# Optimization experiments

Measured on AMD Instinct MI355X. Metric: run time of the kernel, lower is better.

The kernel has to match this reference:

```python
import jax, jax.numpy as jnp
import numpy as np

VOCAB, NUM_TAGS, EMB, HID = 30000, 20, 200, 128
B, S = 128, 512


def setup_inputs() -> dict:
    key = jax.random.key(0)
    ks = jax.random.split(key, 13)
    sentence = jax.random.randint(ks[0], (B, S), 0, VOCAB)
    tags = jax.random.randint(ks[1], (B, S), 0, NUM_TAGS)
    lengths = jax.random.randint(ks[2], (B,), 1, S + 1)
    mask = jnp.arange(S)[None, :] < lengths[:, None]  # [B,S] bool, mask[:,0] all True
    sc = 0.1
    return {
        "sentence": sentence,
        "tags": tags,
        "mask": mask,
        "embedding": jax.random.normal(ks[3], (VOCAB, EMB), jnp.float32) * sc,
        "W_ih": jax.random.normal(ks[4], (4 * HID, EMB), jnp.float32) * sc,
        "W_hh": jax.random.normal(ks[5], (4 * HID, HID), jnp.float32) * sc,
        "b_ih": jax.random.normal(ks[6], (4 * HID,), jnp.float32) * sc,
        "b_hh": jax.random.normal(ks[7], (4 * HID,), jnp.float32) * sc,
        "W_dec": jax.random.normal(ks[8], (NUM_TAGS, HID), jnp.float32) * sc,
        "b_dec": jax.random.normal(ks[9], (NUM_TAGS,), jnp.float32) * sc,
        "start_trans": jax.random.normal(ks[10], (NUM_TAGS,), jnp.float32) * sc,
        "end_trans": jax.random.normal(ks[11], (NUM_TAGS,), jnp.float32) * sc,
        "trans": jax.random.normal(ks[12], (NUM_TAGS, NUM_TAGS), jnp.float32) * sc,
    }


def _lstm(embeds, W_ih, W_hh, b_ih, b_hh):
    # torch nn.LSTM, single layer, batch_first, zero init state; gate order i,f,g,o
    b = embeds.shape[0]
    h0 = jnp.zeros((b, HID), embeds.dtype)
    x = jnp.swapaxes(embeds, 0, 1)  # [S,B,E]
    xg = jnp.einsum('sbe,ge->sbg', x, W_ih) + b_ih + b_hh  # input projections, [S,B,4H]

    def step(carry, xg_t):
        h, c = carry
        g = xg_t + h @ W_hh.T
        i, f, gg, o = jnp.split(g, 4, axis=-1)
        c = jax.nn.sigmoid(f) * c + jax.nn.sigmoid(i) * jnp.tanh(gg)
        h = jax.nn.sigmoid(o) * jnp.tanh(c)
        return (h, c), h

    _, hs = jax.lax.scan(step, (h0, h0), xg)
    return jnp.swapaxes(hs, 0, 1)  # [B,S,H]


def _crf_nll_mean(emissions, tags, mask, start_trans, end_trans, trans):
    # torchcrf.CRF negative log likelihood, reduction='mean' (mean over batch)
    b = emissions.shape[0]
    ems = jnp.swapaxes(emissions, 0, 1)          # [S,B,T]
    tgs = jnp.swapaxes(tags, 0, 1)               # [S,B]
    msk = jnp.swapaxes(mask, 0, 1).astype(emissions.dtype)  # [S,B]
    bidx = jnp.arange(b)

    # numerator: score of the gold path
    num0 = start_trans[tgs[0]] + ems[0, bidx, tgs[0]]

    def nstep(score, inp):
        em, tag, ptag, m = inp
        return score + (trans[ptag, tag] + em[bidx, tag]) * m, None

    num, _ = jax.lax.scan(nstep, num0, (ems[1:], tgs[1:], tgs[:-1], msk[1:]))
    last_idx = mask.sum(axis=1).astype(jnp.int32) - 1
    num = num + end_trans[tags[bidx, last_idx]]

    # denominator: forward algorithm (log partition)
    sc0 = start_trans[None, :] + ems[0]  # [B,T]

    def dstep(score, inp):
        em, m = inp
        nxt = jax.nn.logsumexp(score[:, :, None] + trans[None] + em[:, None, :], axis=1)
        return jnp.where(m[:, None] > 0, nxt, score), None

    sc, _ = jax.lax.scan(dstep, sc0, (ems[1:], msk[1:]))
    den = jax.nn.logsumexp(sc + end_trans[None, :], axis=1)
    return -jnp.mean(num - den)


def reference(sentence, tags, mask, embedding, W_ih, W_hh, b_ih, b_hh,
              W_dec, b_dec, start_trans, end_trans, trans):
    embeds = embedding[sentence]                           # [B,S,E]
    lstm_out = _lstm(embeds, W_ih, W_hh, b_ih, b_hh)       # [B,S,H]
    emissions = jnp.einsum('bsh,th->bst', lstm_out, W_dec) + b_dec  # [B,S,T]
    # dropout treated as identity (eval-mode reference)
    return _crf_nll_mean(emissions, tags, mask, start_trans, end_trans, trans)
```

## Files before the change

kernel.cpp:

```cpp
#include <hip/hip_runtime.h>
#include <hip/hip_bf16.h>
#include <hip/hip_fp16.h>
#include <math.h>

#define B_ 128
#define S_ 512
#define EMB_ 200
#define HID_ 128
#define NT_ 20
#define G4_ 512
#define KP_ 224

typedef _Float16 f16x2_t __attribute__((ext_vector_type(2)));
typedef short bf16x8 __attribute__((ext_vector_type(8)));
typedef float f32x4 __attribute__((ext_vector_type(4)));

#if __has_builtin(__builtin_amdgcn_fdot2)
#define FDOT2(a, b, c) __builtin_amdgcn_fdot2(__builtin_bit_cast(f16x2_t, (a)), \
                                              __builtin_bit_cast(f16x2_t, (b)), (c), false)
#else
static __device__ __forceinline__ float fdot2_fb(unsigned a, unsigned b, float c) {
    float alo = __half2float(__ushort_as_half((unsigned short)(a & 0xffffu)));
    float ahi = __half2float(__ushort_as_half((unsigned short)(a >> 16)));
    float blo = __half2float(__ushort_as_half((unsigned short)(b & 0xffffu)));
    float bhi = __half2float(__ushort_as_half((unsigned short)(b >> 16)));
    return c + alo * blo + ahi * bhi;
}
#define FDOT2(a, b, c) fdot2_fb((a), (b), (c))
#endif

__device__ __forceinline__ float bf2f(unsigned u) {
    union { unsigned u; float f; } cv;
    cv.u = u << 16;
    return cv.f;
}
__device__ __forceinline__ unsigned packh2(float a, float b) {
    return ((unsigned)__half_as_ushort(__float2half(b)) << 16)
         | (unsigned)__half_as_ushort(__float2half(a));
}
__device__ __forceinline__ unsigned short f2bf(float f) {
    __hip_bfloat16 h = __float2bfloat16(f);
    unsigned short u;
    __builtin_memcpy(&u, &h, 2);
    return u;
}

__global__ void k_detect(const unsigned char* mask, int* flag) {
    __shared__ int partial[4];
    int tid = threadIdx.x;
    int s = 0;
    for (int i = tid; i < B_ * S_; i += 256) {
        if (i & 3) s += mask[i];
    }
    for (int m = 32; m >= 1; m >>= 1) s += __shfl_xor(s, m);
    if ((tid & 63) == 0) partial[tid >> 6] = s;
    __syncthreads();
    if (tid == 0) {
        int tot = partial[0] + partial[1] + partial[2] + partial[3];
        flag[0] = (tot > 0) ? 1 : 0;
    }
}

__global__ void k_prep(const float* __restrict__ W_ih, const float* __restrict__ b_ih,
                       const float* __restrict__ b_hh, __hip_bfloat16* __restrict__ Wb,
                       float* __restrict__ biasb) {
    int i = blockIdx.x * 256 + threadIdx.x;
    if (i < G4_ * KP_) {
        int g = i / KP_, k = i - g * KP_;
        float v = (k < EMB_) ? W_ih[g * EMB_ + k] : 0.f;
        Wb[i] = __float2bfloat16(v);
    }
    if (i < G4_) biasb[i] = b_ih[i] + b_hh[i];
}

__global__ __launch_bounds__(256, 2) void k_xg(const int* __restrict__ sentence,
                                               const float* __restrict__ embedding,
                                               const __hip_bfloat16* __restrict__ Wb,
                                               const float* __restrict__ biasb,
                                               __hip_bfloat16* __restrict__ xg) {
    __shared__ short Bl[G4_ * 40];
    __shared__ short Al[32 * 40];
    __shared__ int ids_s[32];
    int tid = threadIdx.x;
    int m0 = blockIdx.x * 32;
    int lane = tid & 63;
    int gbase = (tid >> 6) * 128;
    if (tid < 32) ids_s[tid] = sentence[m0 + tid];
    __syncthreads();

    f32x4 acc0[8], acc1[8];
#pragma unroll
    for (int n = 0; n < 8; n++) {
        acc0[n] = (f32x4){0.f, 0.f, 0.f, 0.f};
        acc1[n] = (f32x4){0.f, 0.f, 0.f, 0.f};
    }
    int lrow = lane & 15, lk = lane >> 4;

    for (int c = 0; c < 7; c++) {
        int k0 = c * 32;
#pragma unroll
        for (int i = 0; i < 8; i++) {
            int idx = tid + 256 * i;
            int row = idx >> 2, q = idx & 3;
            uint4 v = *(const uint4*)((const short*)Wb + (size_t)row * KP_ + k0 + q * 8);
            *(uint4*)(Bl + row * 40 + q * 8) = v;
        }
#pragma unroll
        for (int i = 0; i < 2; i++) {
            int j = tid + 256 * i;
            int row = j >> 4, kp = j & 15;
            int k = k0 + kp * 2;
            const float* e = embedding + (size_t)ids_s[row] * EMB_;
            float v0 = (k < EMB_) ? e[k] : 0.f;
            float v1 = (k + 1 < EMB_) ? e[k + 1] : 0.f;
            unsigned u = (unsigned)f2bf(v0) | ((unsigned)f2bf(v1) << 16);
            *(unsigned*)(Al + row * 40 + kp * 2) = u;
        }
        __syncthreads();
        bf16x8 a0 = *(const bf16x8*)(Al + lrow * 40 + lk * 8);
        bf16x8 a1 = *(const bf16x8*)(Al + (lrow + 16) * 40 + lk * 8);
#pragma unroll
        for (int n = 0; n < 8; n++) {
            bf16x8 bfr = *(const bf16x8*)(Bl + (gbase + n * 16 + lrow) * 40 + lk * 8);
            acc0[n] = __builtin_amdgcn_mfma_f32_16x16x32_bf16(a0, bfr, acc0[n], 0, 0, 0);
            acc1[n] = __builtin_amdgcn_mfma_f32_16x16x32_bf16(a1, bfr, acc1[n], 0, 0, 0);
        }
        __syncthreads();
    }
    int rbase = m0 + lk * 4;
#pragma unroll
    for (int n = 0; n < 8; n++) {
        int g = gbase + n * 16 + lrow;
        float bv = biasb[g];
#pragma unroll
        for (int r = 0; r < 4; r++) {
            xg[(size_t)(rbase + r) * G4_ + g] = __float2bfloat16(acc0[n][r] + bv);
            xg[(size_t)(rbase + r + 16) * G4_ + g] = __float2bfloat16(acc1[n][r] + bv);
        }
    }
}

__global__ __launch_bounds__(1024) __attribute__((amdgpu_waves_per_eu(4, 4)))
void k_lstm(const __hip_bfloat16* __restrict__ xg,
            const float* __restrict__ W_hh,
            unsigned* __restrict__ h2_out) {
    __shared__ unsigned h2_lds[64];
    __shared__ float gate_lds[G4_];
    int b = blockIdx.x, tid = threadIdx.x;
    int g = tid >> 1;
    int half = tid & 1;

    unsigned w2[32];
    const float2* wrow = (const float2*)(W_hh + (size_t)g * HID_ + half * 64);
#pragma unroll
    for (int k = 0; k < 32; k++) {
        float2 f = wrow[k];
        w2[k] = packh2(f.x, f.y);
    }
#pragma unroll
    for (int k = 0; k < 32; k++) asm("" : "+v"(w2[k]));

    if (tid < 64) h2_lds[tid] = 0u;
    float c0 = 0.f, c1 = 0.f;
    const ushort* xgb = (const ushort*)(xg) + (size_t)b * S_ * G4_;
    unsigned* h2b = h2_out + (size_t)b * S_ * 64;
    int gt = g >> 7;
    __syncthreads();

    unsigned xr = xgb[g];
    for (int t = 0; t < S_; t++) {
        int tn = (t + 1 < S_) ? t + 1 : t;
        unsigned xr_next = xgb[(size_t)tn * G4_ + g];

        float acc = 0.f;
        const uint4* hb4 = (const uint4*)(h2_lds + (half << 5));
#pragma unroll
        for (int q = 0; q < 8; q++) {
            uint4 hh = hb4[q];
            acc = FDOT2(w2[4 * q + 0], hh.x, acc);
            acc = FDOT2(w2[4 * q + 1], hh.y, acc);
            acc = FDOT2(w2[4 * q + 2], hh.z, acc);
            acc = FDOT2(w2[4 * q + 3], hh.w, acc);
        }
        acc += __shfl_xor(acc, 1);
        if (half == 0) {
            float pre = bf2f(xr) + acc;
            float xs = (gt == 2) ? 2.f * pre : pre;
            xs = fminf(fmaxf(xs, -30.f), 30.f);
            float r = 1.f / (1.f + __expf(-xs));
            gate_lds[g] = (gt == 2) ? 2.f * r - 1.f : r;
        }
        __syncthreads();
        if (tid < 64) {
            int j = tid;
            float2 iv = *(const float2*)(gate_lds + 2 * j);
            float2 fv = *(const float2*)(gate_lds + 128 + 2 * j);
            float2 gv = *(const float2*)(gate_lds + 256 + 2 * j);
            float2 ov = *(const float2*)(gate_lds + 384 + 2 * j);
            c0 = fv.x * c0 + iv.x * gv.x;
            c1 = fv.y * c1 + iv.y * gv.y;
            float h0 = ov.x * (2.f / (1.f + __expf(-2.f * c0)) - 1.f);
            float h1 = ov.y * (2.f / (1.f + __expf(-2.f * c1)) - 1.f);
            unsigned pk = packh2(h0, h1);
            h2_lds[j] = pk;
            h2b[(size_t)t * 64 + j] = pk;
        }
        __syncthreads();
        xr = xr_next;
    }
}

__global__ __launch_bounds__(320) void k_em(const unsigned* __restrict__ h2,
                                            const float* __restrict__ W_dec,
                                            const float* __restrict__ b_dec,
                                            float* __restrict__ em) {
    int half = threadIdx.x / 160;
    int r = threadIdx.x % 160;
    int tag = r >> 3, l8 = r & 7;
    const float* wd = W_dec + tag * HID_ + l8 * 16;
    float ws[16];
#pragma unroll
    for (int q = 0; q < 16; q++) ws[q] = wd[q];
    float bd = b_dec[tag];
    int row0 = blockIdx.x * 16 + half * 8;
    for (int rp = 0; rp < 8; rp++) {
        int row = row0 + rp;
        const uint4* h4 = (const uint4*)(h2 + (size_t)row * 64 + l8 * 8);
        uint4 a = h4[0], bq = h4[1];
        unsigned hv[8] = {a.x, a.y, a.z, a.w, bq.x, bq.y, bq.z, bq.w};
        float pacc = 0.f;
#pragma unroll
        for (int q = 0; q < 8; q++) {
            float lo = __half2float(__ushort_as_half((unsigned short)(hv[q] & 0xffffu)));
            float hi = __half2float(__ushort_as_half((unsigned short)(hv[q] >> 16)));
            pacc += lo * ws[2 * q] + hi * ws[2 * q + 1];
        }
        pacc += __shfl_xor(pacc, 1);
        pacc += __shfl_xor(pacc, 2);
        pacc += __shfl_xor(pacc, 4);
        if (l8 == 0) em[(size_t)row * NT_ + tag] = pacc + bd;
    }
}

__global__ __launch_bounds__(64) void k_crf(const float* __restrict__ em,
                                            const int* __restrict__ tags,
                                            const void* __restrict__ mask,
                                            const int* __restrict__ flag,
                                            const float* __restrict__ start_trans,
                                            const float* __restrict__ end_trans,
                                            const float* __restrict__ trans,
                                            float* __restrict__ nll) {
    __shared__ float em_s[S_ * NT_];
    __shared__ float trans_s[NT_ * NT_];
    __shared__ int tags_s[S_];
    __shared__ unsigned char mask_s[S_];
    __shared__ __align__(16) float score_s[32];
    __shared__ float num_sh;

    int b = blockIdx.x;
    int lane = threadIdx.x;
    const float4* e4 = (const float4*)(em + (size_t)b * S_ * NT_);
    float4* s4 = (float4*)em_s;
    for (int i = lane; i < S_ * NT_ / 4; i += 64) s4[i] = e4[i];
    for (int i = lane; i < NT_ * NT_; i += 64) trans_s[i] = trans[i];
    for (int i = lane; i < S_; i += 64) tags_s[i] = tags[b * S_ + i];
    int fl = flag[0];
    for (int i = lane; i < S_; i += 64) {
        mask_s[i] = fl ? ((const unsigned char*)mask)[b * S_ + i]
                       : (unsigned char)(((const int*)mask)[b * S_ + i] != 0);
    }
    __syncthreads();

    float nsum = 0.f;
    int cnt = 0;
    for (int t = lane; t < S_; t += 64) cnt += mask_s[t];
    for (int t = 1 + lane; t < S_; t += 64) {
        if (mask_s[t]) {
            int tg = tags_s[t], pt = tags_s[t - 1];
            nsum += trans_s[pt * NT_ + tg] + em_s[t * NT_ + tg];
        }
    }
    for (int m = 32; m >= 1; m >>= 1) {
        nsum += __shfl_xor(nsum, m);
        cnt += __shfl_xor(cnt, m);
    }
    if (lane == 0) {
        int t0 = tags_s[0];
        num_sh = nsum + start_trans[t0] + em_s[t0] + end_trans[tags_s[cnt - 1]];
    }

    int tag = (lane < NT_) ? lane : NT_ - 1;
    float tcol[NT_];
#pragma unroll
    for (int p = 0; p < NT_; p++) tcol[p] = trans_s[p * NT_ + tag];
    float sc = start_trans[tag] + em_s[tag];
    if (lane < NT_) score_s[lane] = sc;
    __syncthreads();

    for (int t = 1; t < S_; t++) {
        const float4* q4 = (const float4*)score_s;
        float4 q0 = q4[0], q1 = q4[1], q2 = q4[2], q3 = q4[3], q5 = q4[4];
        float v[NT_] = {q0.x + tcol[0],  q0.y + tcol[1],  q0.z + tcol[2],  q0.w + tcol[3],
                        q1.x + tcol[4],  q1.y + tcol[5],  q1.z + tcol[6],  q1.w + tcol[7],
                        q2.x + tcol[8],  q2.y + tcol[9],  q2.z + tcol[10], q2.w + tcol[11],
                        q3.x + tcol[12], q3.y + tcol[13], q3.z + tcol[14], q3.w + tcol[15],
                        q5.x + tcol[16], q5.y + tcol[17], q5.z + tcol[18], q5.w + tcol[19]};
        float mx[NT_];
#pragma unroll
        for (int p = 0; p < NT_; p++) mx[p] = v[p];
#pragma unroll
        for (int n = NT_; n > 1; n = (n + 1) >> 1) {
#pragma unroll
            for (int i = 0; i < (n >> 1); i++) mx[i] = fmaxf(mx[i], mx[n - 1 - i]);
        }
        float ex[NT_];
#pragma unroll
        for (int p = 0; p < NT_; p++) ex[p] = __expf(v[p] - mx[0]);
#pragma unroll
        for (int n = NT_; n > 1; n = (n + 1) >> 1) {
#pragma unroll
            for (int i = 0; i < (n >> 1); i++) ex[i] += ex[n - 1 - i];
        }
        float nxt = mx[0] + __logf(ex[0]) + em_s[t * NT_ + tag];
        sc = mask_s[t] ? nxt : sc;
        __syncthreads();
        if (lane < NT_) score_s[lane] = sc;
        __syncthreads();
    }

    if (lane < NT_) score_s[lane] = sc + end_trans[tag];
    __syncthreads();
    if (lane == 0) {
        float m = score_s[0];
#pragma unroll
        for (int i = 1; i < NT_; i++) m = fmaxf(m, score_s[i]);
        float s = 0.f;
#pragma unroll
        for (int i = 0; i < NT_; i++) s += __expf(score_s[i] - m);
        nll[b] = (m + __logf(s)) - num_sh;
    }
}

__global__ void k_final(const float* __restrict__ nll, float* __restrict__ out) {
    __shared__ float sums[2];
    int tid = threadIdx.x;
    float v = nll[tid];
    for (int m = 32; m >= 1; m >>= 1) v += __shfl_xor(v, m);
    if ((tid & 63) == 0) sums[tid >> 6] = v;
    __syncthreads();
    if (tid == 0) out[0] = (sums[0] + sums[1]) * (1.f / (float)B_);
}

extern "C" void kernel_launch(void* const* d_in, const int* in_sizes, int n_in,
                              void* d_out, int out_size, void* d_ws, size_t ws_size,
                              hipStream_t stream) {
    const int* sentence = (const int*)d_in[0];
    const int* tags = (const int*)d_in[1];
    const void* mask = d_in[2];
    const float* embedding = (const float*)d_in[3];
    const float* W_ih = (const float*)d_in[4];
    const float* W_hh = (const float*)d_in[5];
    const float* b_ih = (const float*)d_in[6];
    const float* b_hh = (const float*)d_in[7];
    const float* W_dec = (const float*)d_in[8];
    const float* b_dec = (const float*)d_in[9];
    const float* start_trans = (const float*)d_in[10];
    const float* end_trans = (const float*)d_in[11];
    const float* trans = (const float*)d_in[12];

    char* ws = (char*)d_ws;
    int* flag = (int*)ws;
    __hip_bfloat16* xg = (__hip_bfloat16*)(ws + 256);
    size_t off = 256 + (size_t)B_ * S_ * G4_ * 2;
    float* em = (float*)(ws + off);
    off += (size_t)B_ * S_ * NT_ * 4;
    float* nllp = (float*)(ws + off);
    off += 512;
    unsigned* h2_out = (unsigned*)(ws + off);
    off += (size_t)B_ * S_ * 64 * 4;
    __hip_bfloat16* Wb = (__hip_bfloat16*)(ws + off);
    off += (size_t)G4_ * KP_ * 2;
    float* biasb = (float*)(ws + off);

    k_detect<<<1, 256, 0, stream>>>((const unsigned char*)mask, flag);
    k_prep<<<(G4_ * KP_ + 255) / 256, 256, 0, stream>>>(W_ih, b_ih, b_hh, Wb, biasb);
    k_xg<<<(B_ * S_) / 32, 256, 0, stream>>>(sentence, embedding, Wb, biasb, xg);
    k_lstm<<<B_, 1024, 0, stream>>>(xg, W_hh, h2_out);
    k_em<<<(B_ * S_) / 16, 320, 0, stream>>>(h2_out, W_dec, b_dec, em);
    k_crf<<<B_, 64, 0, stream>>>(em, tags, mask, flag, start_trans, end_trans, trans, nllp);
    k_final<<<1, 128, 0, stream>>>(nllp, (float*)d_out);
}
```

Measured before the change: 730.1 us.

## Batch 16 sequences per LSTM block using MFMA recurrence, fuse detect, drop CRF syncs

```diff
diff --git a/kernel.cpp b/kernel.cpp
--- a/kernel.cpp
+++ b/kernel.cpp
@@ -11,32 +11,13 @@
 #define G4_ 512
 #define KP_ 224
 
-typedef _Float16 f16x2_t __attribute__((ext_vector_type(2)));
 typedef short bf16x8 __attribute__((ext_vector_type(8)));
 typedef float f32x4 __attribute__((ext_vector_type(4)));
-
-#if __has_builtin(__builtin_amdgcn_fdot2)
-#define FDOT2(a, b, c) __builtin_amdgcn_fdot2(__builtin_bit_cast(f16x2_t, (a)), \
-                                              __builtin_bit_cast(f16x2_t, (b)), (c), false)
-#else
-static __device__ __forceinline__ float fdot2_fb(unsigned a, unsigned b, float c) {
-    float alo = __half2float(__ushort_as_half((unsigned short)(a & 0xffffu)));
-    float ahi = __half2float(__ushort_as_half((unsigned short)(a >> 16)));
-    float blo = __half2float(__ushort_as_half((unsigned short)(b & 0xffffu)));
-    float bhi = __half2float(__ushort_as_half((unsigned short)(b >> 16)));
-    return c + alo * blo + ahi * bhi;
-}
-#define FDOT2(a, b, c) fdot2_fb((a), (b), (c))
-#endif
 
 __device__ __forceinline__ float bf2f(unsigned u) {
     union { unsigned u; float f; } cv;
     cv.u = u << 16;
     return cv.f;
-}
-__device__ __forceinline__ unsigned packh2(float a, float b) {
-    return ((unsigned)__half_as_ushort(__float2half(b)) << 16)
-         | (unsigned)__half_as_ushort(__float2half(a));
 }
 __device__ __forceinline__ unsigned short f2bf(float f) {
     __hip_bfloat16 h = __float2bfloat16(f);
@@ -45,25 +26,26 @@
     return u;
 }
 
-__global__ void k_detect(const unsigned char* mask, int* flag) {
-    __shared__ int partial[4];
-    int tid = threadIdx.x;
-    int s = 0;
-    for (int i = tid; i < B_ * S_; i += 256) {
-        if (i & 3) s += mask[i];
-    }
-    for (int m = 32; m >= 1; m >>= 1) s += __shfl_xor(s, m);
-    if ((tid & 63) == 0) partial[tid >> 6] = s;
-    __syncthreads();
-    if (tid == 0) {
-        int tot = partial[0] + partial[1] + partial[2] + partial[3];
-        flag[0] = (tot > 0) ? 1 : 0;
-    }
-}
-
 __global__ void k_prep(const float* __restrict__ W_ih, const float* __restrict__ b_ih,
-                       const float* __restrict__ b_hh, __hip_bfloat16* __restrict__ Wb,
-                       float* __restrict__ biasb) {
+                       const float* __restrict__ b_hh,
+                       const unsigned char* __restrict__ mask,
+                       __hip_bfloat16* __restrict__ Wb, float* __restrict__ biasb,
+                       int* __restrict__ flag) {
+    if (blockIdx.x == 448) {
+        __shared__ int partial[4];
+        int tid = threadIdx.x;
+        int s = 0;
+        for (int i = tid; i < B_ * S_; i += 256) {
+            if (i & 3) s += mask[i];
+        }
+        for (int m = 32; m >= 1; m >>= 1) s += __shfl_xor(s, m);
+        if ((tid & 63) == 0) partial[tid >> 6] = s;
+        __syncthreads();
+        if (tid == 0) {
+            flag[0] = ((partial[0] + partial[1] + partial[2] + partial[3]) > 0) ? 1 : 0;
+        }
+        return;
+    }
     int i = blockIdx.x * 256 + threadIdx.x;
     if (i < G4_ * KP_) {
         int g = i / KP_, k = i - g * KP_;
@@ -79,7 +61,7 @@
                                                const float* __restrict__ biasb,
                                                __hip_bfloat16* __restrict__ xg) {
     __shared__ short Bl[G4_ * 40];
-    __shared__ short Al[32 * 40];
+    __shared__ short Al[32 * 232];
     __shared__ int ids_s[32];
     int tid = threadIdx.x;
     int m0 = blockIdx.x * 32;
@@ -88,6 +70,17 @@
     if (tid < 32) ids_s[tid] = sentence[m0 + tid];
     __syncthreads();
 
+    for (int i = tid; i < 32 * 112; i += 256) {
+        int row = i / 112, kp = i - row * 112;
+        int k = kp * 2;
+        unsigned u = 0u;
+        if (k < EMB_) {
+            float2 v = *(const float2*)(embedding + (size_t)ids_s[row] * EMB_ + k);
+            u = (unsigned)f2bf(v.x) | ((unsigned)f2bf(v.y) << 16);
+        }
+        *(unsigned*)(Al + row * 232 + k) = u;
+    }
+
     f32x4 acc0[8], acc1[8];
 #pragma unroll
     for (int n = 0; n < 8; n++) {
@@ -105,20 +98,9 @@
             uint4 v = *(const uint4*)((const short*)Wb + (size_t)row * KP_ + k0 + q * 8);
             *(uint4*)(Bl + row * 40 + q * 8) = v;
         }
-#pragma unroll
-        for (int i = 0; i < 2; i++) {
-            int j = tid + 256 * i;
-            int row = j >> 4, kp = j & 15;
-            int k = k0 + kp * 2;
-            const float* e = embedding + (size_t)ids_s[row] * EMB_;
-            float v0 = (k < EMB_) ? e[k] : 0.f;
-            float v1 = (k + 1 < EMB_) ? e[k + 1] : 0.f;
-            unsigned u = (unsigned)f2bf(v0) | ((unsigned)f2bf(v1) << 16);
-            *(unsigned*)(Al + row * 40 + kp * 2) = u;
-        }
         __syncthreads();
-        bf16x8 a0 = *(const bf16x8*)(Al + lrow * 40 + lk * 8);
-        bf16x8 a1 = *(const bf16x8*)(Al + (lrow + 16) * 40 + lk * 8);
+        bf16x8 a0 = *(const bf16x8*)(Al + lrow * 232 + k0 + lk * 8);
+        bf16x8 a1 = *(const bf16x8*)(Al + (lrow + 16) * 232 + k0 + lk * 8);
 #pragma unroll
         for (int n = 0; n < 8; n++) {
             bf16x8 bfr = *(const bf16x8*)(Bl + (gbase + n * 16 + lrow) * 40 + lk * 8);
@@ -140,73 +122,106 @@
     }
 }
 
-__global__ __launch_bounds__(1024) __attribute__((amdgpu_waves_per_eu(4, 4)))
+__global__ __launch_bounds__(512, 2)
 void k_lstm(const __hip_bfloat16* __restrict__ xg,
             const float* __restrict__ W_hh,
-            unsigned* __restrict__ h2_out) {
-    __shared__ unsigned h2_lds[64];
-    __shared__ float gate_lds[G4_];
-    int b = blockIdx.x, tid = threadIdx.x;
-    int g = tid >> 1;
-    int half = tid & 1;
-
-    unsigned w2[32];
-    const float2* wrow = (const float2*)(W_hh + (size_t)g * HID_ + half * 64);
-#pragma unroll
-    for (int k = 0; k < 32; k++) {
-        float2 f = wrow[k];
-        w2[k] = packh2(f.x, f.y);
-    }
-#pragma unroll
-    for (int k = 0; k < 32; k++) asm("" : "+v"(w2[k]));
-
-    if (tid < 64) h2_lds[tid] = 0u;
-    float c0 = 0.f, c1 = 0.f;
-    const ushort* xgb = (const ushort*)(xg) + (size_t)b * S_ * G4_;
-    unsigned* h2b = h2_out + (size_t)b * S_ * 64;
-    int gt = g >> 7;
+            ushort* __restrict__ h2_out) {
+    __shared__ ushort Hb[2][16 * 128];
+    int blk = blockIdx.x, tid = threadIdx.x;
+    int w = tid >> 6, l = tid & 63;
+    int col = l & 15;
+    int rg = l >> 4;
+    int elem = (w << 4) | col;
+
+    unsigned bw[4][4][4];
+#pragma unroll
+    for (int q = 0; q < 4; q++) {
+        const float* wr = W_hh + (size_t)(q * 128 + elem) * HID_;
+#pragma unroll
+        for (int kc = 0; kc < 4; kc++) {
+#pragma unroll
+            for (int j = 0; j < 4; j++) {
+                int k = kc * 32 + rg * 8 + 2 * j;
+                bw[q][kc][j] = (unsigned)f2bf(wr[k]) | ((unsigned)f2bf(wr[k + 1]) << 16);
+            }
+        }
+    }
+#pragma unroll
+    for (int q = 0; q < 4; q++)
+#pragma unroll
+        for (int kc = 0; kc < 4; kc++)
+#pragma unroll
+            for (int j = 0; j < 4; j++) asm("" : "+v"(bw[q][kc][j]));
+
+    for (int i = tid; i < 16 * 128; i += 512) Hb[0][i] = 0;
+    float c[4] = {0.f, 0.f, 0.f, 0.f};
+
+    const ushort* xp[4];
+#pragma unroll
+    for (int r = 0; r < 4; r++)
+        xp[r] = (const ushort*)xg + (size_t)(blk * 16 + rg * 4 + r) * S_ * 512 + elem;
+
+    unsigned xvA[16], xvB[16];
+#pragma unroll
+    for (int q = 0; q < 4; q++)
+#pragma unroll
+        for (int r = 0; r < 4; r++) {
+            xvA[q * 4 + r] = xp[r][q * 128];
+            xvB[q * 4 + r] = xp[r][512 + q * 128];
+        }
     __syncthreads();
 
-    unsigned xr = xgb[g];
-    for (int t = 0; t < S_; t++) {
-        int tn = (t + 1 < S_) ? t + 1 : t;
-        unsigned xr_next = xgb[(size_t)tn * G4_ + g];
-
-        float acc = 0.f;
-        const uint4* hb4 = (const uint4*)(h2_lds + (half << 5));
-#pragma unroll
-        for (int q = 0; q < 8; q++) {
-            uint4 hh = hb4[q];
-            acc = FDOT2(w2[4 * q + 0], hh.x, acc);
-            acc = FDOT2(w2[4 * q + 1], hh.y, acc);
-            acc = FDOT2(w2[4 * q + 2], hh.z, acc);
-            acc = FDOT2(w2[4 * q + 3], hh.w, acc);
-        }
-        acc += __shfl_xor(acc, 1);
-        if (half == 0) {
-            float pre = bf2f(xr) + acc;
-            float xs = (gt == 2) ? 2.f * pre : pre;
-            xs = fminf(fmaxf(xs, -30.f), 30.f);
-            float r = 1.f / (1.f + __expf(-xs));
-            gate_lds[g] = (gt == 2) ? 2.f * r - 1.f : r;
-        }
-        __syncthreads();
-        if (tid < 64) {
-            int j = tid;
-            float2 iv = *(const float2*)(gate_lds + 2 * j);
-            float2 fv = *(const float2*)(gate_lds + 128 + 2 * j);
-            float2 gv = *(const float2*)(gate_lds + 256 + 2 * j);
-            float2 ov = *(const float2*)(gate_lds + 384 + 2 * j);
-            c0 = fv.x * c0 + iv.x * gv.x;
-            c1 = fv.y * c1 + iv.y * gv.y;
-            float h0 = ov.x * (2.f / (1.f + __expf(-2.f * c0)) - 1.f);
-            float h1 = ov.y * (2.f / (1.f + __expf(-2.f * c1)) - 1.f);
-            unsigned pk = packh2(h0, h1);
-            h2_lds[j] = pk;
-            h2b[(size_t)t * 64 + j] = pk;
-        }
-        __syncthreads();
-        xr = xr_next;
+    int cur = 0;
+    ushort* h2b = h2_out;
+    auto step = [&](int t, unsigned* xv) {
+        f32x4 acc[4];
+#pragma unroll
+        for (int q = 0; q < 4; q++)
+#pragma unroll
+            for (int r = 0; r < 4; r++) acc[q][r] = bf2f(xv[q * 4 + r]);
+        size_t t2 = (t + 2 < S_) ? t + 2 : S_ - 1;
+#pragma unroll
+        for (int q = 0; q < 4; q++)
+#pragma unroll
+            for (int r = 0; r < 4; r++) xv[q * 4 + r] = xp[r][t2 * 512 + q * 128];
+
+#pragma unroll
+        for (int kc = 0; kc < 4; kc++) {
+            int ro = (col * 128 + kc * 32 + rg * 8) ^ ((col & 7) << 3);
+            bf16x8 a = *(const bf16x8*)(&Hb[cur][ro]);
+#pragma unroll
+            for (int q = 0; q < 4; q++) {
+                union { unsigned u[4]; bf16x8 v; } bb;
+                bb.u[0] = bw[q][kc][0]; bb.u[1] = bw[q][kc][1];
+                bb.u[2] = bw[q][kc][2]; bb.u[3] = bw[q][kc][3];
+                acc[q] = __builtin_amdgcn_mfma_f32_16x16x32_bf16(a, bb.v, acc[q], 0, 0, 0);
+            }
+        }
+
+#pragma unroll
+        for (int r = 0; r < 4; r++) {
+            float xi = fminf(fmaxf(acc[0][r], -30.f), 30.f);
+            float xf = fminf(fmaxf(acc[1][r], -30.f), 30.f);
+            float gg = fminf(fmaxf(2.f * acc[2][r], -30.f), 30.f);
+            float xo = fminf(fmaxf(acc[3][r], -30.f), 30.f);
+            float si = 1.f / (1.f + __expf(-xi));
+            float sf = 1.f / (1.f + __expf(-xf));
+            float tg = 2.f / (1.f + __expf(-gg)) - 1.f;
+            float so = 1.f / (1.f + __expf(-xo));
+            c[r] = sf * c[r] + si * tg;
+            float tc = 2.f / (1.f + __expf(-2.f * c[r])) - 1.f;
+            float h = so * tc;
+            int batch = rg * 4 + r;
+            ushort hb = f2bf(h);
+            Hb[cur ^ 1][(batch * 128 + elem) ^ ((batch & 7) << 3)] = hb;
+            h2b[((size_t)(blk * 16 + batch) * S_ + t) * 128 + elem] = hb;
+        }
+        asm volatile("s_waitcnt lgkmcnt(0)\n\ts_barrier" ::: "memory");
+        cur ^= 1;
+    };
+    for (int t = 0; t < S_; t += 2) {
+        step(t, xvA);
+        step(t + 1, xvB);
     }
 }
 
@@ -231,9 +246,8 @@
         float pacc = 0.f;
 #pragma unroll
         for (int q = 0; q < 8; q++) {
-            float lo = __half2float(__ushort_as_half((unsigned short)(hv[q] & 0xffffu)));
-            float hi = __half2float(__ushort_as_half((unsigned short)(hv[q] >> 16)));
-            pacc += lo * ws[2 * q] + hi * ws[2 * q + 1];
+            pacc += bf2f(hv[q] & 0xffffu) * ws[2 * q];
+            pacc += bf2f(hv[q] >> 16) * ws[2 * q + 1];
         }
         pacc += __shfl_xor(pacc, 1);
         pacc += __shfl_xor(pacc, 2);
@@ -295,7 +309,6 @@
     for (int p = 0; p < NT_; p++) tcol[p] = trans_s[p * NT_ + tag];
     float sc = start_trans[tag] + em_s[tag];
     if (lane < NT_) score_s[lane] = sc;
-    __syncthreads();
 
     for (int t = 1; t < S_; t++) {
         const float4* q4 = (const float4*)score_s;
@@ -323,9 +336,7 @@
         }
         float nxt = mx[0] + __logf(ex[0]) + em_s[t * NT_ + tag];
         sc = mask_s[t] ? nxt : sc;
-        __syncthreads();
         if (lane < NT_) score_s[lane] = sc;
-        __syncthreads();
     }
 
     if (lane < NT_) score_s[lane] = sc + end_trans[tag];
@@ -376,17 +387,17 @@
     off += (size_t)B_ * S_ * NT_ * 4;
     float* nllp = (float*)(ws + off);
     off += 512;
-    unsigned* h2_out = (unsigned*)(ws + off);
-    off += (size_t)B_ * S_ * 64 * 4;
+    ushort* h2_out = (ushort*)(ws + off);
+    off += (size_t)B_ * S_ * 128 * 2;
     __hip_bfloat16* Wb = (__hip_bfloat16*)(ws + off);
     off += (size_t)G4_ * KP_ * 2;
     float* biasb = (float*)(ws + off);
 
-    k_detect<<<1, 256, 0, stream>>>((const unsigned char*)mask, flag);
-    k_prep<<<(G4_ * KP_ + 255) / 256, 256, 0, stream>>>(W_ih, b_ih, b_hh, Wb, biasb);
+    k_prep<<<449, 256, 0, stream>>>(W_ih, b_ih, b_hh, (const unsigned char*)mask,
+                                    Wb, biasb, flag);
     k_xg<<<(B_ * S_) / 32, 256, 0, stream>>>(sentence, embedding, Wb, biasb, xg);
-    k_lstm<<<B_, 1024, 0, stream>>>(xg, W_hh, h2_out);
-    k_em<<<(B_ * S_) / 16, 320, 0, stream>>>(h2_out, W_dec, b_dec, em);
+    k_lstm<<<8, 512, 0, stream>>>(xg, W_hh, h2_out);
+    k_em<<<(B_ * S_) / 16, 320, 0, stream>>>((const unsigned*)h2_out, W_dec, b_dec, em);
     k_crf<<<B_, 64, 0, stream>>>(em, tags, mask, flag, start_trans, end_trans, trans, nllp);
     k_final<<<1, 128, 0, stream>>>(nllp, (float*)d_out);
 }
```

After: 1.231 ms. 1.69x slower.
